# Optimization experiments

Measured on AMD Instinct MI355X. Metric: run time of the kernel, lower is better.

## Reference

```python
import jax, jax.numpy as jnp
import numpy as np
from jax import lax

# hyperparams (match init_kwargs)
DIM = 192      # dim
QK = 192       # qk_dim
HEADS = 8
GS = 128       # group_size
MLP = 384      # mlp_dim
M = 64         # num_tokens
B, H, W = 4, 128, 128


def setup_inputs() -> dict:
    key = jax.random.key(0)
    ks = jax.random.split(key, 12)
    def n(k, sh, sc=0.02):
        return jax.random.normal(k, sh, dtype=jnp.float32) * sc
    return {
        "x": n(ks[0], (B, DIM, H, W), 1.0),
        "ln_g": jnp.ones((DIM,), jnp.float32),
        "ln_b": jnp.zeros((DIM,), jnp.float32),
        "Wq": n(ks[1], (DIM, QK)),
        "Wk": n(ks[2], (DIM, QK)),
        "Wv": n(ks[3], (DIM, DIM)),
        "Wproj": n(ks[4], (DIM, DIM)),
        "Wkg": n(ks[5], (DIM, QK)),      # IRCA global-key projection of means
        "Wvg": n(ks[6], (DIM, DIM)),     # IRCA global-value projection of means
        "means": n(ks[7], (M, DIM), 1.0),  # token dictionary buffer
        "Wconv": n(ks[8], (DIM, DIM)),   # 1x1 conv (no bias) as matrix
        "mlp_ln_g": jnp.ones((DIM,), jnp.float32),
        "mlp_ln_b": jnp.zeros((DIM,), jnp.float32),
        "W_fc1": n(ks[9], (DIM, MLP)),
        "dw": n(ks[10], (MLP, 1, 3, 3)),  # depthwise 3x3 in ConvFFN
        "W_fc2": n(ks[11], (MLP, DIM)),
    }


def _ln(x, g, b, eps=1e-5):
    mu = x.mean(-1, keepdims=True)
    var = ((x - mu) ** 2).mean(-1, keepdims=True)
    return (x - mu) * lax.rsqrt(var + eps) * g + b


def _attn(q, k, v):
    scale = q.shape[-1] ** -0.5
    s = jnp.einsum('...qd,...kd->...qk', q, k) * scale
    p = jax.nn.softmax(s, axis=-1)
    return jnp.einsum('...qk,...kd->...qd', p, v)


def reference(x, ln_g, ln_b, Wq, Wk, Wv, Wproj, Wkg, Wvg, means,
              Wconv, mlp_ln_g, mlp_ln_b, W_fc1, dw, W_fc2):
    b, C, h, w = x.shape
    N = h * w
    xt = x.reshape(b, C, N).transpose(0, 2, 1)          # b n c
    residual = xt
    xn = _ln(xt, ln_g, ln_b)

    # IRCA: per-head global K/V from the token dictionary (means)
    kg = (means @ Wkg).reshape(M, HEADS, QK // HEADS).transpose(1, 0, 2)   # h m dq
    vg = (means @ Wvg).reshape(M, HEADS, C // HEADS).transpose(1, 0, 2)    # h m dv

    # cluster assignment (no-grad): cosine sim to means, argsort by cluster id
    xs = lax.stop_gradient(xn)
    ms = lax.stop_gradient(means)
    xs_n = xs / (jnp.linalg.norm(xs, axis=-1, keepdims=True) + 1e-12)
    ms_n = ms / (jnp.linalg.norm(ms, axis=-1, keepdims=True) + 1e-12)
    belong = jnp.argmax(xs_n @ ms_n.T, axis=-1)          # b n
    idx = jnp.argsort(belong, axis=-1)                   # b n, cluster-sorted order

    # IASA: project, gather into cluster-sorted order
    q = jnp.take_along_axis(xn @ Wq, idx[:, :, None], axis=1)
    k = jnp.take_along_axis(xn @ Wk, idx[:, :, None], axis=1)
    v = jnp.take_along_axis(xn @ Wv, idx[:, :, None], axis=1)

    gs = min(N, GS)
    ng = (N + gs - 1) // gs
    pad_n = ng * gs - N
    pq = jnp.concatenate([q, q[:, N - pad_n:N][:, ::-1]], axis=1)
    pq = pq.reshape(b, ng, gs, HEADS, -1).transpose(0, 1, 3, 2, 4)  # b ng h gs dq

    def windows(t):
        tr = jnp.concatenate([t, t[:, N - pad_n - gs:N][:, ::-1]], axis=1)  # len ng*gs+gs
        t1 = tr[:, :ng * gs].reshape(b, ng, gs, -1)
        t2 = tr[:, gs:].reshape(b, ng, gs, -1)
        tw = jnp.concatenate([t1, t2], axis=2)           # b ng 2gs c
        return tw.reshape(b, ng, 2 * gs, HEADS, -1).transpose(0, 1, 3, 2, 4)

    kw, vw = windows(k), windows(v)
    out1 = _attn(pq, kw, vw)                             # local overlapping windows
    out2 = _attn(pq, kg[None, None], vg[None, None])     # global dictionary attention
    out = (out1 + out2).transpose(0, 1, 3, 2, 4).reshape(b, ng * gs, C)[:, :N]

    # scatter back to original token order (idx is a permutation)
    inv = jnp.argsort(idx, axis=-1)
    out = jnp.take_along_axis(out, inv[:, :, None], axis=1)
    out = (out @ Wproj) @ Wconv                           # proj + 1x1 conv (no bias)
    xt = residual + out

    # PreNorm ConvFFN: LN -> fc1 -> depthwise 3x3 -> GELU -> fc2, residual
    h1 = _ln(xt, mlp_ln_g, mlp_ln_b) @ W_fc1              # b n mlp
    himg = h1.transpose(0, 2, 1).reshape(b, MLP, h, w)
    dwc = lax.conv_general_dilated(himg, dw, (1, 1), 'SAME',
                                   feature_group_count=MLP,
                                   dimension_numbers=('NCHW', 'OIHW', 'NCHW'))
    h2 = jax.nn.gelu(dwc.reshape(b, MLP, N).transpose(0, 2, 1))
    xt = xt + h2 @ W_fc2
    return xt.transpose(0, 2, 1).reshape(b, C, h, w)
```

## Files before the change

### kernel.cpp

```cpp
#include <hip/hip_runtime.h>

using u16 = unsigned short;
using u32 = unsigned int;
typedef __attribute__((ext_vector_type(8))) short short8;
typedef __attribute__((ext_vector_type(4))) short s16x4;
typedef __attribute__((ext_vector_type(4))) float f32x4;
typedef __attribute__((ext_vector_type(2))) float f32x2;
typedef __attribute__((ext_vector_type(4))) u16 u16x4;
typedef __attribute__((ext_vector_type(4))) u32 u32x4;

constexpr int CB   = 4;
constexpr int CC   = 192;
constexpr int CN   = 16384;
constexpr int BN   = CB * CN;
constexpr int CMLP = 384;

__device__ __forceinline__ float b2f(u16 u){ return __uint_as_float(((u32)u) << 16); }
__device__ __forceinline__ u16 f2b(float f){
  u32 u = __float_as_uint(f);
  u32 r = (u + 0x7FFFu + ((u >> 16) & 1u)) >> 16;
  return (u16)r;
}
__device__ __forceinline__ short8 ld8(const u16* p) {
  s16x4 a = *(const s16x4*)p;
  s16x4 b = *(const s16x4*)(p + 4);
  short8 r;
  r[0]=a[0]; r[1]=a[1]; r[2]=a[2]; r[3]=a[3];
  r[4]=b[0]; r[5]=b[1]; r[6]=b[2]; r[7]=b[3];
  return r;
}
__device__ __forceinline__ u32 pk_bf16(float lo, float hi) {
  u32 r;
  asm("v_cvt_pk_bf16_f32 %0, %1, %2" : "=v"(r) : "v"(lo), "v"(hi));
  return r;
}
__device__ __forceinline__ float exp2_fast(float x) {
  float r;
  asm("v_exp_f32 %0, %1" : "=v"(r) : "v"(x));
  return r;
}
__device__ __forceinline__ void gl_lds16(const u16* g, u16* l) {
  __builtin_amdgcn_global_load_lds(
      (const __attribute__((address_space(1))) void*)(const void*)g,
      (__attribute__((address_space(3))) void*)(void*)l, 16, 0, 0);
}

template<int DOARG>
__global__ __launch_bounds__(256) void ln_k(const float* __restrict__ src,
    const float* __restrict__ gg, const float* __restrict__ bb, u16* __restrict__ out,
    const u16* __restrict__ msnT, int* __restrict__ belong)
{
  __shared__ float t[64 * 193];
  __shared__ float sg[192], sb[192];
  __shared__ float smu[64], srs[64];
  const int tid = threadIdx.x;
  const int blk = blockIdx.x;
  const int b = blk >> 8;
  const int n0 = (blk & 255) * 64;
  if (tid < 192) { sg[tid] = gg[tid]; sb[tid] = bb[tid]; }
  const size_t sbase = ((size_t)b * CC) * CN + n0;
  #pragma unroll
  for (int it = 0; it < 48; ++it) {
    int c = it * 4 + (tid >> 6);
    int tok = tid & 63;
    t[tok * 193 + c] = src[sbase + (size_t)c * CN + tok];
  }
  __syncthreads();
  {
    int tok = tid >> 2, sub = tid & 3;
    float s = 0.f, sq = 0.f;
    #pragma unroll
    for (int i = 0; i < 48; ++i) {
      float v = t[tok * 193 + sub * 48 + i];
      s += v; sq += v * v;
    }
    s  += __shfl_xor(s, 1);  s  += __shfl_xor(s, 2);
    sq += __shfl_xor(sq, 1); sq += __shfl_xor(sq, 2);
    float mu = s * (1.f / 192.f);
    float var = fmaxf(sq * (1.f / 192.f) - mu * mu, 0.f);
    float rs = rsqrtf(var + 1e-5f);
    if (sub == 0) { smu[tok] = mu; srs[tok] = rs; }
  }
  __syncthreads();
  const size_t obase = ((size_t)(b * CN + n0)) * CC;
  #pragma unroll
  for (int it = 0; it < 48; ++it) {
    int e = it * 256 + tid;
    int tk = e / 192, c = e % 192;
    float v = (t[tk * 193 + c] - smu[tk]) * srs[tk] * sg[c] + sb[c];
    out[obase + (size_t)tk * CC + c] = f2b(v);
  }

  if (DOARG) {
    const int wv = tid >> 6, lane = tid & 63;
    const int l15 = lane & 15, g4 = lane >> 4, q8 = g4 * 8;
    const int tok = wv * 16 + l15;
    const float mu = smu[tok], rs = srs[tok];
    short8 afm[6];
    #pragma unroll
    for (int ks = 0; ks < 6; ++ks) {
      u32x4 qq;
      #pragma unroll
      for (int j = 0; j < 4; ++j) {
        int c = ks * 32 + q8 + 2 * j;
        float v0 = (t[tok * 193 + c]     - mu) * rs * sg[c]     + sb[c];
        float v1 = (t[tok * 193 + c + 1] - mu) * rs * sg[c + 1] + sb[c + 1];
        qq[j] = pk_bf16(v0, v1);
      }
      afm[ks] = __builtin_bit_cast(short8, qq);
    }
    f32x4 sacc[4];
    #pragma unroll
    for (int ct = 0; ct < 4; ++ct) {
      sacc[ct] = 0.f;
      const u16* pM = msnT + (ct * 16 + l15) * 192 + q8;
      short8 mf[6];
      #pragma unroll
      for (int ks = 0; ks < 6; ++ks) mf[ks] = *(const short8*)(pM + ks * 32);
      #pragma unroll
      for (int ks = 0; ks < 6; ++ks)
        sacc[ct] = __builtin_amdgcn_mfma_f32_16x16x32_bf16(afm[ks], mf[ks], sacc[ct], 0, 0, 0);
    }
    #pragma unroll
    for (int r = 0; r < 4; ++r) {
      float bv = -3e38f; int bi = 1 << 30;
      #pragma unroll
      for (int ct = 0; ct < 4; ++ct) {
        float v = sacc[ct][r];
        int ci = ct * 16 + l15;
        if (v > bv || (v == bv && ci < bi)) { bv = v; bi = ci; }
      }
      #pragma unroll
      for (int d = 1; d < 16; d <<= 1) {
        float ov = __shfl_xor(bv, d);
        int   oi = __shfl_xor(bi, d);
        if (ov > bv || (ov == bv && oi < bi)) { bv = ov; bi = oi; }
      }
      if (l15 == 0) belong[b * CN + n0 + wv * 16 + g4 * 4 + r] = bi;
    }
  }
}

__global__ __launch_bounds__(192) void prep_means_k(const float* __restrict__ means,
    const float* __restrict__ Wkg, const float* __restrict__ Wvg,
    u16* __restrict__ msnT, float* __restrict__ kg, float* __restrict__ vg)
{
  __shared__ float sv[192];
  __shared__ float red[192];
  const int m = blockIdx.x, c = threadIdx.x;
  float v = means[m * 192 + c];
  sv[c] = v; red[c] = v * v;
  __syncthreads();
  for (int s = 96; s >= 3; s >>= 1) {
    if (c < s) red[c] += red[c + s];
    __syncthreads();
  }
  if (c == 0) red[0] = 1.f / (sqrtf(red[0] + red[1] + red[2]) + 1e-12f);
  __syncthreads();
  float scale = red[0];
  msnT[m * 192 + c] = f2b(v * scale);
  float a1 = 0.f, a2 = 0.f;
  for (int cc = 0; cc < 192; ++cc) {
    float mv = sv[cc];
    a1 += mv * Wkg[cc * 192 + c];
    a2 += mv * Wvg[cc * 192 + c];
  }
  int h = c / 24, d = c % 24;
  kg[h * (64 * 24) + m * 24 + d] = a1;
  vg[h * (64 * 24) + m * 24 + d] = a2;
}

__global__ __launch_bounds__(256) void wprep_k(
    const float* __restrict__ Wp, const float* __restrict__ Wc, u16* __restrict__ WpcT,
    const float* __restrict__ Wq, const float* __restrict__ Wk, const float* __restrict__ Wv,
    u16* __restrict__ WqkvT,
    const float* __restrict__ Wfc1, u16* __restrict__ Wfc1T,
    const float* __restrict__ Wfc2, u16* __restrict__ Wfc2T)
{
  int blk = blockIdx.x;
  int tid = threadIdx.x;
  if (blk < 144) {
    int e = blk * 256 + tid;
    if (e < 192 * 192) {
      int i = e / 192, j = e % 192;
      float a = 0.f;
      for (int k = 0; k < 192; ++k) a += Wp[i * 192 + k] * Wc[k * 192 + j];
      WpcT[j * 192 + i] = f2b(a);
    }
    return;
  }
  blk -= 144;
  if (blk < 432) {
    int which = blk / 144;
    int e = (blk % 144) * 256 + tid;
    const float* W = (which == 0) ? Wq : (which == 1) ? Wk : Wv;
    if (e < 192 * 192) {
      int j = e / 192, k = e % 192;
      WqkvT[which * 192 * 192 + e] = f2b(W[k * 192 + j]);
    }
    return;
  }
  blk -= 432;
  if (blk < 288) {
    int e = blk * 256 + tid;
    if (e < 192 * 384) {
      int j = e / 192, k = e % 192;
      Wfc1T[e] = f2b(Wfc1[k * 384 + j]);
    }
    return;
  }
  blk -= 288;
  {
    int e = blk * 256 + tid;
    if (e < 384 * 192) {
      int j = e / 384, k = e % 384;
      Wfc2T[e] = f2b(Wfc2[k * 192 + j]);
    }
  }
}

enum { EP_QKV = 0, EP_RESID = 2, EP_H1 = 3, EP_FINAL = 4 };

template<int KTOT, int NCOLS, int EPI>
__global__ __launch_bounds__(256) void gemm3_k(const u16* __restrict__ A,
    const u16* __restrict__ Wt, const void* __restrict__ residp,
    void* __restrict__ outp, int astride,
    const float* __restrict__ g2, const float* __restrict__ b2, u16* __restrict__ ln2out)
{
  constexpr bool LNB = (EPI == EP_RESID);
  constexpr size_t SH_BYTES = LNB ? (size_t)(64 * 197 * 4) : (size_t)(64 * 192 * 2);
  __shared__ __attribute__((aligned(16))) char shraw[SH_BYTES];
  __shared__ float smu2[64], srs2[64];
  u16*   lA    = (u16*)shraw;
  float* lnbuf = (float*)shraw;
  constexpr int KC = KTOT / 192;
  constexpr int WCOLS = NCOLS / 4;
  constexpr int WCT = WCOLS / 16;
  constexpr int NACC = (KC == 2) ? WCT * 4 : 4;
  const int tid = threadIdx.x;
  const int row0 = blockIdx.y * 64;
  const int b = row0 >> 14;
  const int col0 = blockIdx.x * NCOLS;
  const int wv = tid >> 6, lane = tid & 63;
  const int l15 = lane & 15, g4 = lane >> 4, q8 = g4 * 8;
  const int colw = col0 + wv * WCOLS;

  f32x4 acc[NACC];
  #pragma unroll
  for (int i = 0; i < NACC; ++i) acc[i] = 0.f;

  #pragma unroll
  for (int kc = 0; kc < KC; ++kc) {
    if (kc) __syncthreads();
    #pragma unroll
    for (int j = 0; j < 6; ++j) {
      int C = (wv * 6 + j) * 64 + lane;
      int r = C / 24;
      int c = C - r * 24;
      const u16* gp = A + (size_t)(row0 + r) * astride + kc * 192 + c * 8;
      gl_lds16(gp, lA + (wv * 6 + j) * 512);
    }
    __syncthreads();
    short8 af[4][6];
    #pragma unroll
    for (int rt = 0; rt < 4; ++rt)
      #pragma unroll
      for (int ks = 0; ks < 6; ++ks)
        af[rt][ks] = *(const short8*)(lA + (rt * 16 + l15) * 192 + ks * 32 + q8);
    if (LNB) __syncthreads();

    #pragma unroll
    for (int jc = 0; jc < WCT; ++jc) {
      const u16* pW = Wt + (size_t)(colw + jc * 16 + l15) * KTOT + kc * 192 + q8;
      short8 wf[6];
      #pragma unroll
      for (int ks = 0; ks < 6; ++ks) wf[ks] = *(const short8*)(pW + ks * 32);
      #pragma unroll
      for (int ks = 0; ks < 6; ++ks)
        #pragma unroll
        for (int rt = 0; rt < 4; ++rt) {
          int ai = (KC == 2) ? jc * 4 + rt : rt;
          if (EPI == EP_FINAL || EPI == EP_RESID)
            acc[ai] = __builtin_amdgcn_mfma_f32_16x16x32_bf16(wf[ks], af[rt][ks], acc[ai], 0, 0, 0);
          else
            acc[ai] = __builtin_amdgcn_mfma_f32_16x16x32_bf16(af[rt][ks], wf[ks], acc[ai], 0, 0, 0);
        }

      if (KC == 1 && EPI == EP_QKV) {
        u16* o = (u16*)outp;
        int col = colw + jc * 16 + l15;
        #pragma unroll
        for (int rt = 0; rt < 4; ++rt) {
          int row = row0 + rt * 16 + g4 * 4;
          #pragma unroll
          for (int r = 0; r < 4; ++r)
            o[(size_t)(row + r) * 576 + col] = f2b(acc[rt][r]);
          acc[rt] = 0.f;
        }
      } else if (KC == 1 && EPI == EP_H1) {
        u16* o = (u16*)outp;
        int col = colw + jc * 16 + l15;
        #pragma unroll
        for (int rt = 0; rt < 4; ++rt) {
          int row = row0 + rt * 16 + g4 * 4;
          #pragma unroll
          for (int r = 0; r < 4; ++r)
            o[(size_t)(row + r) * CMLP + col] = f2b(acc[rt][r]);
          acc[rt] = 0.f;
        }
      } else if (KC == 1 && EPI == EP_RESID) {
        const float* resid = (const float*)residp;
        u16* o = (u16*)outp;
        #pragma unroll
        for (int rt = 0; rt < 4; ++rt) {
          int n = ((row0 + rt * 16) & 16383) + l15;
          #pragma unroll
          for (int r = 0; r < 4; ++r) {
            int col = colw + jc * 16 + g4 * 4 + r;
            size_t o2 = ((size_t)(b * CC + col)) * CN + n;
            float val = resid[o2] + acc[rt][r];
            o[o2] = f2b(val);
            lnbuf[(rt * 16 + l15) * 197 + col] = val;
          }
          acc[rt] = 0.f;
        }
      }
    }
  }

  if (EPI == EP_RESID) {
    __syncthreads();
    {
      int tok = tid >> 2, sub = tid & 3;
      float s = 0.f, sq = 0.f;
      #pragma unroll
      for (int i = 0; i < 48; ++i) {
        float v = lnbuf[tok * 197 + sub * 48 + i];
        s += v; sq += v * v;
      }
      s  += __shfl_xor(s, 1);  s  += __shfl_xor(s, 2);
      sq += __shfl_xor(sq, 1); sq += __shfl_xor(sq, 2);
      float mu = s * (1.f / 192.f);
      float var = fmaxf(sq * (1.f / 192.f) - mu * mu, 0.f);
      float rs = rsqrtf(var + 1e-5f);
      if (sub == 0) { smu2[tok] = mu; srs2[tok] = rs; }
    }
    __syncthreads();
    const size_t obase = (size_t)row0 * CC;
    #pragma unroll
    for (int it = 0; it < 48; ++it) {
      int e = it * 256 + tid;
      int tk = e / 192, c = e % 192;
      float v = (lnbuf[tk * 197 + c] - smu2[tk]) * srs2[tk] * g2[c] + b2[c];
      ln2out[obase + (size_t)tk * CC + c] = f2b(v);
    }
  } else if (EPI == EP_FINAL) {
    const u16* resid = (const u16*)residp;
    float* o = (float*)outp;
    #pragma unroll
    for (int jc = 0; jc < WCT; ++jc)
      #pragma unroll
      for (int tt = 0; tt < 4; ++tt) {
        int n = ((row0 + tt * 16) & 16383) + l15;
        #pragma unroll
        for (int r = 0; r < 4; ++r) {
          int outcol = colw + jc * 16 + g4 * 4 + r;
          size_t o2 = ((size_t)(b * CC + outcol)) * CN + n;
          o[o2] = b2f(resid[o2]) + acc[jc * 4 + tt][r];
        }
      }
  }
}

__global__ __launch_bounds__(256) void hist_k(const int* __restrict__ belong, int* __restrict__ histG)
{
  __shared__ int h[64];
  int tid = threadIdx.x, blk = blockIdx.x;
  if (tid < 64) h[tid] = 0;
  __syncthreads();
  int c = belong[blk * 256 + tid];
  atomicAdd(&h[c], 1);
  __syncthreads();
  if (tid < 64) histG[blk * 64 + tid] = h[tid];
}

__global__ __launch_bounds__(64) void scan_k(const int* __restrict__ histG, int* __restrict__ chunkBase)
{
  int b = blockIdx.x, c = threadIdx.x;
  int tot = 0;
  for (int ch = 0; ch < 64; ++ch) tot += histG[(b * 64 + ch) * 64 + c];
  int inc = tot;
  for (int d = 1; d < 64; d <<= 1) {
    int v = __shfl_up(inc, d);
    if (c >= d) inc += v;
  }
  int run = inc - tot;
  for (int ch = 0; ch < 64; ++ch) {
    chunkBase[(b * 64 + ch) * 64 + c] = run;
    run += histG[(b * 64 + ch) * 64 + c];
  }
}

__global__ __launch_bounds__(256) void rank_k(const int* __restrict__ belong,
    const int* __restrict__ chunkBase, int* __restrict__ idx)
{
  __shared__ int WH[4][64];
  int tid = threadIdx.x, blk = blockIdx.x;
  int b = blk >> 6, chl = blk & 63;
  int wv = tid >> 6, lane = tid & 63;
  ((int*)WH)[tid] = 0;
  __syncthreads();
  int nl = chl * 256 + tid;
  int c = belong[blk * 256 + tid];
  int rank = 0;
  for (int m = 0; m < 64; ++m) {
    unsigned long long msk = __ballot(c == m);
    if (c == m) {
      rank = __popcll(msk & ((1ull << lane) - 1ull));
      if (rank == 0) WH[wv][m] = __popcll(msk);
    }
  }
  __syncthreads();
  int off = 0;
  #pragma unroll
  for (int w = 0; w < 3; ++w) if (w < wv) off += WH[w][c];
  int pos = chunkBase[(b * 64 + chl) * 64 + c] + off + rank;
  idx[b * CN + pos] = nl;
}

__global__ __launch_bounds__(256) void attn_k(u16* __restrict__ qkv,
    const float* __restrict__ kg, const float* __restrict__ vg,
    const int* __restrict__ idx)
{
  __shared__ __attribute__((aligned(16))) u16 sK[320 * 24];
  __shared__ __attribute__((aligned(16))) u16 sVT[25 * 332];
  __shared__ u16 sidx[256];
  const int g = blockIdx.x, h = blockIdx.y, b = blockIdx.z;
  const int tid = threadIdx.x;
  const int wave = tid >> 6, lane = tid & 63;
  const int l15 = lane & 15, g4 = lane >> 4;
  const int q8 = g4 * 8;
  const size_t base = (size_t)b * CN * 576;
  const float QSC = 0.20412414523193154f * 1.4426950408889634f;
  short8 z8 = {0,0,0,0,0,0,0,0};

  {
    int p = g * 128 + tid;
    if (p >= CN) p = 2 * CN - 1 - p;
    sidx[tid] = (u16)idx[b * CN + p];
  }
  for (int e = tid; e < 332; e += 256) sVT[24 * 332 + e] = 0x3F80;
  __syncthreads();

  #pragma unroll
  for (int it = 0; it < 8; ++it) {
    int e4 = (it * 256 + tid) * 4;
    if (e4 < 7680) {
      int r = e4 / 24, c = e4 % 24;
      if (r < 256) {
        int p = sidx[r];
        *(u16x4*)(sK + r * 24 + c) =
          *(const u16x4*)(qkv + base + (size_t)p * 576 + 192 + h * 24 + c);
      } else {
        const float* kp = kg + h * 1536 + (r - 256) * 24 + c;
        u16x4 o;
        o[0] = f2b(kp[0]); o[1] = f2b(kp[1]); o[2] = f2b(kp[2]); o[3] = f2b(kp[3]);
        *(u16x4*)(sK + r * 24 + c) = o;
      }
    }
  }
  #pragma unroll
  for (int it = 0; it < 8; ++it) {
    int e4 = (it * 256 + tid) * 4;
    if (e4 < 7680) {
      int kk = e4 / 24, c = e4 % 24;
      if (kk < 256) {
        int p = sidx[kk];
        u16x4 v = *(const u16x4*)(qkv + base + (size_t)p * 576 + 384 + h * 24 + c);
        sVT[(c + 0) * 332 + kk] = v[0];
        sVT[(c + 1) * 332 + kk] = v[1];
        sVT[(c + 2) * 332 + kk] = v[2];
        sVT[(c + 3) * 332 + kk] = v[3];
      } else {
        const float* vp = vg + h * 1536 + (kk - 256) * 24 + c;
        sVT[(c + 0) * 332 + kk] = f2b(vp[0]);
        sVT[(c + 1) * 332 + kk] = f2b(vp[1]);
        sVT[(c + 2) * 332 + kk] = f2b(vp[2]);
        sVT[(c + 3) * 332 + kk] = f2b(vp[3]);
      }
    }
  }

  short8 qf[2];
  #pragma unroll
  for (int rt = 0; rt < 2; ++rt) {
    int qrow = sidx[wave * 32 + rt * 16 + l15];
    if (g4 < 3) {
      short8 raw = ld8(qkv + base + (size_t)qrow * 576 + h * 24 + q8);
      u32x4 qq;
      #pragma unroll
      for (int j = 0; j < 4; ++j) {
        float lo = b2f((u16)raw[2 * j]) * QSC;
        float hi = b2f((u16)raw[2 * j + 1]) * QSC;
        qq[j] = pk_bf16(lo, hi);
      }
      qf[rt] = __builtin_bit_cast(short8, qq);
    } else {
      qf[rt] = z8;
    }
  }
  __syncthreads();

  f32x4 O1[2][2], O2[2][2];
  #pragma unroll
  for (int rt = 0; rt < 2; ++rt)
    #pragma unroll
    for (int ct2 = 0; ct2 < 2; ++ct2) { O1[rt][ct2] = 0.f; O2[rt][ct2] = 0.f; }

  const int srcLo = ((lane & 16) << 1) + l15;
  const int srcHi = srcLo + 16;
  const bool hiSel = lane >= 32;
  f32x4 zz = 0.f;

  auto do_tile = [&](int ktile, f32x4 (*O)[2]) {
    short8 aK[4];
    #pragma unroll
    for (int ct = 0; ct < 4; ++ct)
      aK[ct] = (g4 < 3) ? ld8(sK + (ktile + ct * 16 + l15) * 24 + q8) : z8;
    short8 bV[2][2];
    #pragma unroll
    for (int kc = 0; kc < 2; ++kc)
      #pragma unroll
      for (int ct2 = 0; ct2 < 2; ++ct2) {
        int vrow = ct2 * 16 + l15;
        bV[kc][ct2] = (vrow < 25) ? ld8(sVT + vrow * 332 + ktile + kc * 32 + q8) : z8;
      }
    #pragma unroll
    for (int rt = 0; rt < 2; ++rt) {
      f32x4 p[4];
      __builtin_amdgcn_s_setprio(1);
      #pragma unroll
      for (int ct = 0; ct < 4; ++ct)
        p[ct] = __builtin_amdgcn_mfma_f32_16x16x32_bf16(aK[ct], qf[rt], zz, 0, 0, 0);
      __builtin_amdgcn_s_setprio(0);
      #pragma unroll
      for (int ct = 0; ct < 4; ++ct)
        #pragma unroll
        for (int r = 0; r < 4; ++r)
          p[ct][r] = exp2_fast(p[ct][r]);
      #pragma unroll
      for (int kc = 0; kc < 2; ++kc) {
        u32 wA0 = pk_bf16(p[kc * 2][0], p[kc * 2][1]);
        u32 wA1 = pk_bf16(p[kc * 2][2], p[kc * 2][3]);
        u32 wB0 = pk_bf16(p[kc * 2 + 1][0], p[kc * 2 + 1][1]);
        u32 wB1 = pk_bf16(p[kc * 2 + 1][2], p[kc * 2 + 1][3]);
        u32 a0 = (u32)__shfl((int)wA0, srcLo), a1 = (u32)__shfl((int)wA1, srcLo);
        u32 a2 = (u32)__shfl((int)wA0, srcHi), a3 = (u32)__shfl((int)wA1, srcHi);
        u32 b0 = (u32)__shfl((int)wB0, srcLo), b1 = (u32)__shfl((int)wB1, srcLo);
        u32 b2 = (u32)__shfl((int)wB0, srcHi), b3 = (u32)__shfl((int)wB1, srcHi);
        u32x4 fr;
        fr[0] = hiSel ? b0 : a0; fr[1] = hiSel ? b1 : a1;
        fr[2] = hiSel ? b2 : a2; fr[3] = hiSel ? b3 : a3;
        short8 aP = __builtin_bit_cast(short8, fr);
        __builtin_amdgcn_s_setprio(1);
        #pragma unroll
        for (int ct2 = 0; ct2 < 2; ++ct2)
          O[rt][ct2] = __builtin_amdgcn_mfma_f32_16x16x32_bf16(aP, bV[kc][ct2], O[rt][ct2], 0, 0, 0);
        __builtin_amdgcn_s_setprio(0);
      }
    }
  };

  do_tile(0,   O1);
  do_tile(64,  O1);
  do_tile(128, O1);
  do_tile(192, O1);
  do_tile(256, O2);

  const int lsrc = (lane & 48) + 8;
  #pragma unroll
  for (int rt = 0; rt < 2; ++rt) {
    #pragma unroll
    for (int r = 0; r < 4; ++r) {
      float s1 = __shfl(O1[rt][1][r], lsrc);
      float s2 = __shfl(O2[rt][1][r], lsrc);
      float i1 = 1.f / s1;
      float i2 = 1.f / s2;
      int tok = sidx[wave * 32 + rt * 16 + g4 * 4 + r];
      #pragma unroll
      for (int ct2 = 0; ct2 < 2; ++ct2) {
        int d = ct2 * 16 + l15;
        if (d < 24) {
          float v = O1[rt][ct2][r] * i1 + O2[rt][ct2][r] * i2;
          qkv[base + (size_t)tok * 576 + h * 24 + d] = f2b(v);
        }
      }
    }
  }
}

__global__ __launch_bounds__(256) void conv_k(const u16* __restrict__ h1,
    const float* __restrict__ dw, u16* __restrict__ h2g)
{
  __shared__ float t[1156 * 10];
  __shared__ float sdw[72];
  const int tile = blockIdx.x;
  const int jg = blockIdx.y;
  const int bb = blockIdx.z;
  const int y0 = (tile >> 2) * 32, x0 = (tile & 3) * 32;
  const int tid = threadIdx.x;
  if (tid < 72) sdw[tid] = dw[jg * 72 + tid];
  #pragma unroll
  for (int it = 0; it < 5; ++it) {
    int e = it * 256 + tid;
    if (e < 1156) {
      int yy = e / 34 - 1 + y0, xx = e % 34 - 1 + x0;
      float v[8];
      if (yy >= 0 && yy < 128 && xx >= 0 && xx < 128) {
        short8 raw = *(const short8*)(h1 + ((size_t)(bb * CN + yy * 128 + xx)) * CMLP + jg * 8);
        #pragma unroll
        for (int c = 0; c < 8; ++c) v[c] = b2f((u16)raw[c]);
      } else {
        #pragma unroll
        for (int c = 0; c < 8; ++c) v[c] = 0.f;
      }
      #pragma unroll
      for (int c = 0; c < 8; c += 2) {
        f32x2 p; p[0] = v[c]; p[1] = v[c + 1];
        *(f32x2*)(t + e * 10 + c) = p;
      }
    }
  }
  __syncthreads();
  float acc[4][8];
  #pragma unroll
  for (int px = 0; px < 4; ++px)
    #pragma unroll
    for (int c = 0; c < 8; ++c) acc[px][c] = 0.f;
  #pragma unroll
  for (int k = 0; k < 9; ++k) {
    const int dy = k / 3, dx = k % 3;
    float w[8];
    #pragma unroll
    for (int c = 0; c < 8; ++c) w[c] = sdw[c * 9 + k];
    #pragma unroll
    for (int px = 0; px < 4; ++px) {
      int idx2 = px * 256 + tid;
      int oy = idx2 >> 5, ox = idx2 & 31;
      const float* vp = t + ((oy + dy) * 34 + ox + dx) * 10;
      #pragma unroll
      for (int c = 0; c < 8; ++c) acc[px][c] += vp[c] * w[c];
    }
  }
  #pragma unroll
  for (int px = 0; px < 4; ++px) {
    int idx2 = px * 256 + tid;
    int oy = idx2 >> 5, ox = idx2 & 31;
    short8 o;
    #pragma unroll
    for (int c = 0; c < 8; ++c) {
      float a = acc[px][c];
      float u = 1.5957691216057308f * (a + 0.044715f * a * a * a);
      float gel = a / (1.f + __expf(-u));
      o[c] = (short)f2b(gel);
    }
    *(short8*)(h2g + ((size_t)(bb * CN + (y0 + oy) * 128 + x0 + ox)) * CMLP + jg * 8) = o;
  }
}

extern "C" void kernel_launch(void* const* d_in, const int* in_sizes, int n_in,
                              void* d_out, int out_size, void* d_ws, size_t ws_size,
                              hipStream_t stream)
{
  const float* x     = (const float*)d_in[0];
  const float* ln_g  = (const float*)d_in[1];
  const float* ln_b  = (const float*)d_in[2];
  const float* Wq    = (const float*)d_in[3];
  const float* Wk    = (const float*)d_in[4];
  const float* Wv    = (const float*)d_in[5];
  const float* Wproj = (const float*)d_in[6];
  const float* Wkg   = (const float*)d_in[7];
  const float* Wvg   = (const float*)d_in[8];
  const float* means = (const float*)d_in[9];
  const float* Wconv = (const float*)d_in[10];
  const float* mlp_g = (const float*)d_in[11];
  const float* mlp_b = (const float*)d_in[12];
  const float* Wfc1  = (const float*)d_in[13];
  const float* dw    = (const float*)d_in[14];
  const float* Wfc2  = (const float*)d_in[15];
  float* out = (float*)d_out;
  (void)in_sizes; (void)n_in; (void)out_size; (void)ws_size;

  char* ws = (char*)d_ws;
  size_t off = 0;
  auto alloc = [&](size_t sz) { void* p = ws + off; off += (sz + 255) & ~(size_t)255; return p; };
  u16*  xn    = (u16*)alloc((size_t)BN * 192 * 2);
  u16*  qkv   = (u16*)alloc((size_t)BN * 576 * 2);
  u16*  xt2   = (u16*)alloc((size_t)BN * 192 * 2);
  u16*  h2g   = (u16*)alloc((size_t)BN * 384 * 2);
  u16*  msnT  = (u16*)alloc(64 * 192 * 2);
  u16*  WqkvT = (u16*)alloc(576 * 192 * 2);
  u16*  WpcT  = (u16*)alloc(192 * 192 * 2);
  u16*  Wfc1T = (u16*)alloc(384 * 192 * 2);
  u16*  Wfc2T = (u16*)alloc(192 * 384 * 2);
  float* kg   = (float*)alloc(8 * 64 * 24 * 4);
  float* vg   = (float*)alloc(8 * 64 * 24 * 4);
  int*  belong = (int*)alloc(BN * 4);
  int*  idxb   = (int*)alloc(BN * 4);
  int*  histG  = (int*)alloc(256 * 64 * 4);
  int*  chunkBase = (int*)alloc(256 * 64 * 4);
  u16* ln2 = xn;
  u16* h1  = qkv;

  prep_means_k<<<64, 192, 0, stream>>>(means, Wkg, Wvg, msnT, kg, vg);
  wprep_k<<<1152, 256, 0, stream>>>(Wproj, Wconv, WpcT, Wq, Wk, Wv, WqkvT,
                                    Wfc1, Wfc1T, Wfc2, Wfc2T);

  ln_k<1><<<1024, 256, 0, stream>>>(x, ln_g, ln_b, xn, msnT, belong);
  hist_k<<<256, 256, 0, stream>>>(belong, histG);
  scan_k<<<4, 64, 0, stream>>>(histG, chunkBase);
  rank_k<<<256, 256, 0, stream>>>(belong, chunkBase, idxb);
  gemm3_k<192, 576, EP_QKV><<<dim3(1, 1024), 256, 0, stream>>>(xn, WqkvT, nullptr, qkv, 192, nullptr, nullptr, nullptr);
  attn_k<<<dim3(128, 8, 4), 256, 0, stream>>>(qkv, kg, vg, idxb);
  gemm3_k<192, 192, EP_RESID><<<dim3(1, 1024), 256, 0, stream>>>(qkv, WpcT, x, xt2, 576, mlp_g, mlp_b, ln2);
  gemm3_k<192, 384, EP_H1><<<dim3(1, 1024), 256, 0, stream>>>(ln2, Wfc1T, nullptr, h1, 192, nullptr, nullptr, nullptr);
  conv_k<<<dim3(16, 48, 4), 256, 0, stream>>>(h1, dw, h2g);
  gemm3_k<384, 192, EP_FINAL><<<dim3(1, 1024), 256, 0, stream>>>(h2g, Wfc2T, xt2, out, 384, nullptr, nullptr, nullptr);
}
```

Before: 319.1 us.

## Fuse LN into QKV GEMM and proj/residual/LN2 into fc1 GEMM

The first LayerNorm kernel now computes the QKV projection directly from its register-resident normalized fragments, so the bf16 normalized activation is no longer written to and reread from global memory. The proj+residual kernel now runs LN2 in shared memory and immediately does the fc1 GEMM, removing the LN2 round trip and one launch. This cuts two kernel launches and roughly two full activation round trips. In exchange, the LN2 statistics are computed from bf16-rounded residual values instead of fp32, and each wave in the QKV step does far more serial MFMA work per block, with weights streamed from global memory.

```diff
diff --git a/kernel.cpp b/kernel.cpp
--- a/kernel.cpp
+++ b/kernel.cpp
@@ -45,10 +45,10 @@
       (__attribute__((address_space(3))) void*)(void*)l, 16, 0, 0);
 }
 
-template<int DOARG>
-__global__ __launch_bounds__(256) void ln_k(const float* __restrict__ src,
-    const float* __restrict__ gg, const float* __restrict__ bb, u16* __restrict__ out,
-    const u16* __restrict__ msnT, int* __restrict__ belong)
+__global__ __launch_bounds__(256) void lnqkv_k(const float* __restrict__ src,
+    const float* __restrict__ gg, const float* __restrict__ bb,
+    const u16* __restrict__ msnT, const u16* __restrict__ WqkvT,
+    int* __restrict__ belong, u16* __restrict__ qkv)
 {
   __shared__ float t[64 * 193];
   __shared__ float sg[192], sb[192];
@@ -82,33 +82,26 @@
     if (sub == 0) { smu[tok] = mu; srs[tok] = rs; }
   }
   __syncthreads();
-  const size_t obase = ((size_t)(b * CN + n0)) * CC;
-  #pragma unroll
-  for (int it = 0; it < 48; ++it) {
-    int e = it * 256 + tid;
-    int tk = e / 192, c = e % 192;
-    float v = (t[tk * 193 + c] - smu[tk]) * srs[tk] * sg[c] + sb[c];
-    out[obase + (size_t)tk * CC + c] = f2b(v);
-  }
-
-  if (DOARG) {
-    const int wv = tid >> 6, lane = tid & 63;
-    const int l15 = lane & 15, g4 = lane >> 4, q8 = g4 * 8;
-    const int tok = wv * 16 + l15;
-    const float mu = smu[tok], rs = srs[tok];
-    short8 afm[6];
-    #pragma unroll
-    for (int ks = 0; ks < 6; ++ks) {
-      u32x4 qq;
-      #pragma unroll
-      for (int j = 0; j < 4; ++j) {
-        int c = ks * 32 + q8 + 2 * j;
-        float v0 = (t[tok * 193 + c]     - mu) * rs * sg[c]     + sb[c];
-        float v1 = (t[tok * 193 + c + 1] - mu) * rs * sg[c + 1] + sb[c + 1];
-        qq[j] = pk_bf16(v0, v1);
-      }
-      afm[ks] = __builtin_bit_cast(short8, qq);
-    }
+
+  const int wv = tid >> 6, lane = tid & 63;
+  const int l15 = lane & 15, g4 = lane >> 4, q8 = g4 * 8;
+  const int tok = wv * 16 + l15;
+  const float mu = smu[tok], rs = srs[tok];
+  short8 afm[6];
+  #pragma unroll
+  for (int ks = 0; ks < 6; ++ks) {
+    u32x4 qq;
+    #pragma unroll
+    for (int j = 0; j < 4; ++j) {
+      int c = ks * 32 + q8 + 2 * j;
+      float v0 = (t[tok * 193 + c]     - mu) * rs * sg[c]     + sb[c];
+      float v1 = (t[tok * 193 + c + 1] - mu) * rs * sg[c + 1] + sb[c + 1];
+      qq[j] = pk_bf16(v0, v1);
+    }
+    afm[ks] = __builtin_bit_cast(short8, qq);
+  }
+
+  {
     f32x4 sacc[4];
     #pragma unroll
     for (int ct = 0; ct < 4; ++ct) {
@@ -138,6 +131,23 @@
       }
       if (l15 == 0) belong[b * CN + n0 + wv * 16 + g4 * 4 + r] = bi;
     }
+  }
+
+  const size_t rowb = (size_t)(b * CN + n0 + wv * 16 + g4 * 4);
+  #pragma unroll 4
+  for (int jc = 0; jc < 36; ++jc) {
+    const u16* pW = WqkvT + (size_t)(jc * 16 + l15) * 192 + q8;
+    short8 wf[6];
+    #pragma unroll
+    for (int ks = 0; ks < 6; ++ks) wf[ks] = *(const short8*)(pW + ks * 32);
+    f32x4 acc = 0.f;
+    #pragma unroll
+    for (int ks = 0; ks < 6; ++ks)
+      acc = __builtin_amdgcn_mfma_f32_16x16x32_bf16(afm[ks], wf[ks], acc, 0, 0, 0);
+    int col = jc * 16 + l15;
+    #pragma unroll
+    for (int r = 0; r < 4; ++r)
+      qkv[(rowb + r) * 576 + col] = f2b(acc[r]);
   }
 }
 
@@ -219,35 +229,145 @@
   }
 }
 
-enum { EP_QKV = 0, EP_RESID = 2, EP_H1 = 3, EP_FINAL = 4 };
-
-template<int KTOT, int NCOLS, int EPI>
-__global__ __launch_bounds__(256) void gemm3_k(const u16* __restrict__ A,
-    const u16* __restrict__ Wt, const void* __restrict__ residp,
-    void* __restrict__ outp, int astride,
-    const float* __restrict__ g2, const float* __restrict__ b2, u16* __restrict__ ln2out)
-{
-  constexpr bool LNB = (EPI == EP_RESID);
-  constexpr size_t SH_BYTES = LNB ? (size_t)(64 * 197 * 4) : (size_t)(64 * 192 * 2);
-  __shared__ __attribute__((aligned(16))) char shraw[SH_BYTES];
+__global__ __launch_bounds__(256) void resid_k(const u16* __restrict__ qkv,
+    const u16* __restrict__ WpcT, const float* __restrict__ x, u16* __restrict__ xt2,
+    const float* __restrict__ g2, const float* __restrict__ b2,
+    const u16* __restrict__ Wfc1T, u16* __restrict__ h1)
+{
+  __shared__ __attribute__((aligned(16))) u16 shraw[64 * 200];
   __shared__ float smu2[64], srs2[64];
-  u16*   lA    = (u16*)shraw;
-  float* lnbuf = (float*)shraw;
+  u16* lA    = shraw;
+  u16* lnb16 = shraw;
+  const int tid = threadIdx.x;
+  const int row0 = blockIdx.x * 64;
+  const int b = row0 >> 14;
+  const int wv = tid >> 6, lane = tid & 63;
+  const int l15 = lane & 15, g4 = lane >> 4, q8 = g4 * 8;
+
+  #pragma unroll
+  for (int j = 0; j < 6; ++j) {
+    int C = (wv * 6 + j) * 64 + lane;
+    int r = C / 24;
+    int c = C - r * 24;
+    const u16* gp = qkv + (size_t)(row0 + r) * 576 + c * 8;
+    gl_lds16(gp, lA + (wv * 6 + j) * 512);
+  }
+  __syncthreads();
+  short8 af[4][6];
+  #pragma unroll
+  for (int rt = 0; rt < 4; ++rt)
+    #pragma unroll
+    for (int ks = 0; ks < 6; ++ks)
+      af[rt][ks] = *(const short8*)(lA + (rt * 16 + l15) * 192 + ks * 32 + q8);
+  __syncthreads();
+
+  const int colw = wv * 48;
+  #pragma unroll
+  for (int jc = 0; jc < 3; ++jc) {
+    const u16* pW = WpcT + (size_t)(colw + jc * 16 + l15) * 192 + q8;
+    short8 wf[6];
+    #pragma unroll
+    for (int ks = 0; ks < 6; ++ks) wf[ks] = *(const short8*)(pW + ks * 32);
+    f32x4 acc[4];
+    #pragma unroll
+    for (int rt = 0; rt < 4; ++rt) acc[rt] = 0.f;
+    #pragma unroll
+    for (int ks = 0; ks < 6; ++ks)
+      #pragma unroll
+      for (int rt = 0; rt < 4; ++rt)
+        acc[rt] = __builtin_amdgcn_mfma_f32_16x16x32_bf16(wf[ks], af[rt][ks], acc[rt], 0, 0, 0);
+    #pragma unroll
+    for (int rt = 0; rt < 4; ++rt) {
+      int n = ((row0 + rt * 16) & 16383) + l15;
+      #pragma unroll
+      for (int r = 0; r < 4; ++r) {
+        int col = colw + jc * 16 + g4 * 4 + r;
+        size_t o2 = ((size_t)(b * CC + col)) * CN + n;
+        float val = x[o2] + acc[rt][r];
+        u16 vb = f2b(val);
+        xt2[o2] = vb;
+        lnb16[(rt * 16 + l15) * 200 + col] = vb;
+      }
+    }
+  }
+  __syncthreads();
+
+  {
+    int tok = tid >> 2, sub = tid & 3;
+    float s = 0.f, sq = 0.f;
+    #pragma unroll
+    for (int i = 0; i < 48; ++i) {
+      float v = b2f(lnb16[tok * 200 + sub * 48 + i]);
+      s += v; sq += v * v;
+    }
+    s  += __shfl_xor(s, 1);  s  += __shfl_xor(s, 2);
+    sq += __shfl_xor(sq, 1); sq += __shfl_xor(sq, 2);
+    float mu = s * (1.f / 192.f);
+    float var = fmaxf(sq * (1.f / 192.f) - mu * mu, 0.f);
+    float rs = rsqrtf(var + 1e-5f);
+    if (sub == 0) { smu2[tok] = mu; srs2[tok] = rs; }
+  }
+  __syncthreads();
+  #pragma unroll
+  for (int it = 0; it < 48; ++it) {
+    int e = it * 256 + tid;
+    int tk = e / 192, c = e % 192;
+    float v = (b2f(lnb16[tk * 200 + c]) - smu2[tk]) * srs2[tk] * g2[c] + b2[c];
+    lnb16[tk * 200 + c] = f2b(v);
+  }
+  __syncthreads();
+
+  short8 af2[4][6];
+  #pragma unroll
+  for (int rt = 0; rt < 4; ++rt)
+    #pragma unroll
+    for (int ks = 0; ks < 6; ++ks)
+      af2[rt][ks] = *(const short8*)(lnb16 + (rt * 16 + l15) * 200 + ks * 32 + q8);
+  const int colw2 = wv * 96;
+  #pragma unroll
+  for (int jc = 0; jc < 6; ++jc) {
+    const u16* pW = Wfc1T + (size_t)(colw2 + jc * 16 + l15) * 192 + q8;
+    short8 wf[6];
+    #pragma unroll
+    for (int ks = 0; ks < 6; ++ks) wf[ks] = *(const short8*)(pW + ks * 32);
+    f32x4 acc[4];
+    #pragma unroll
+    for (int rt = 0; rt < 4; ++rt) acc[rt] = 0.f;
+    #pragma unroll
+    for (int ks = 0; ks < 6; ++ks)
+      #pragma unroll
+      for (int rt = 0; rt < 4; ++rt)
+        acc[rt] = __builtin_amdgcn_mfma_f32_16x16x32_bf16(af2[rt][ks], wf[ks], acc[rt], 0, 0, 0);
+    int col = colw2 + jc * 16 + l15;
+    #pragma unroll
+    for (int rt = 0; rt < 4; ++rt) {
+      int row = row0 + rt * 16 + g4 * 4;
+      #pragma unroll
+      for (int r = 0; r < 4; ++r)
+        h1[(size_t)(row + r) * CMLP + col] = f2b(acc[rt][r]);
+    }
+  }
+}
+
+template<int KTOT, int NCOLS>
+__global__ __launch_bounds__(256) void gemmF_k(const u16* __restrict__ A,
+    const u16* __restrict__ Wt, const u16* __restrict__ resid,
+    float* __restrict__ o, int astride)
+{
+  __shared__ __attribute__((aligned(16))) u16 lA[64 * 192];
   constexpr int KC = KTOT / 192;
   constexpr int WCOLS = NCOLS / 4;
   constexpr int WCT = WCOLS / 16;
-  constexpr int NACC = (KC == 2) ? WCT * 4 : 4;
   const int tid = threadIdx.x;
-  const int row0 = blockIdx.y * 64;
+  const int row0 = blockIdx.x * 64;
   const int b = row0 >> 14;
-  const int col0 = blockIdx.x * NCOLS;
   const int wv = tid >> 6, lane = tid & 63;
   const int l15 = lane & 15, g4 = lane >> 4, q8 = g4 * 8;
-  const int colw = col0 + wv * WCOLS;
-
-  f32x4 acc[NACC];
-  #pragma unroll
-  for (int i = 0; i < NACC; ++i) acc[i] = 0.f;
+  const int colw = wv * WCOLS;
+
+  f32x4 acc[WCT * 4];
+  #pragma unroll
+  for (int i = 0; i < WCT * 4; ++i) acc[i] = 0.f;
 
   #pragma unroll
   for (int kc = 0; kc < KC; ++kc) {
@@ -267,7 +387,6 @@
       #pragma unroll
       for (int ks = 0; ks < 6; ++ks)
         af[rt][ks] = *(const short8*)(lA + (rt * 16 + l15) * 192 + ks * 32 + q8);
-    if (LNB) __syncthreads();
 
     #pragma unroll
     for (int jc = 0; jc < WCT; ++jc) {
@@ -278,98 +397,22 @@
       #pragma unroll
       for (int ks = 0; ks < 6; ++ks)
         #pragma unroll
-        for (int rt = 0; rt < 4; ++rt) {
-          int ai = (KC == 2) ? jc * 4 + rt : rt;
-          if (EPI == EP_FINAL || EPI == EP_RESID)
-            acc[ai] = __builtin_amdgcn_mfma_f32_16x16x32_bf16(wf[ks], af[rt][ks], acc[ai], 0, 0, 0);
-          else
-            acc[ai] = __builtin_amdgcn_mfma_f32_16x16x32_bf16(af[rt][ks], wf[ks], acc[ai], 0, 0, 0);
-        }
-
-      if (KC == 1 && EPI == EP_QKV) {
-        u16* o = (u16*)outp;
-        int col = colw + jc * 16 + l15;
-        #pragma unroll
-        for (int rt = 0; rt < 4; ++rt) {
-          int row = row0 + rt * 16 + g4 * 4;
-          #pragma unroll
-          for (int r = 0; r < 4; ++r)
-            o[(size_t)(row + r) * 576 + col] = f2b(acc[rt][r]);
-          acc[rt] = 0.f;
-        }
-      } else if (KC == 1 && EPI == EP_H1) {
-        u16* o = (u16*)outp;
-        int col = colw + jc * 16 + l15;
-        #pragma unroll
-        for (int rt = 0; rt < 4; ++rt) {
-          int row = row0 + rt * 16 + g4 * 4;
-          #pragma unroll
-          for (int r = 0; r < 4; ++r)
-            o[(size_t)(row + r) * CMLP + col] = f2b(acc[rt][r]);
-          acc[rt] = 0.f;
-        }
-      } else if (KC == 1 && EPI == EP_RESID) {
-        const float* resid = (const float*)residp;
-        u16* o = (u16*)outp;
-        #pragma unroll
-        for (int rt = 0; rt < 4; ++rt) {
-          int n = ((row0 + rt * 16) & 16383) + l15;
-          #pragma unroll
-          for (int r = 0; r < 4; ++r) {
-            int col = colw + jc * 16 + g4 * 4 + r;
-            size_t o2 = ((size_t)(b * CC + col)) * CN + n;
-            float val = resid[o2] + acc[rt][r];
-            o[o2] = f2b(val);
-            lnbuf[(rt * 16 + l15) * 197 + col] = val;
-          }
-          acc[rt] = 0.f;
-        }
-      }
-    }
-  }
-
-  if (EPI == EP_RESID) {
-    __syncthreads();
-    {
-      int tok = tid >> 2, sub = tid & 3;
-      float s = 0.f, sq = 0.f;
-      #pragma unroll
-      for (int i = 0; i < 48; ++i) {
-        float v = lnbuf[tok * 197 + sub * 48 + i];
-        s += v; sq += v * v;
-      }
-      s  += __shfl_xor(s, 1);  s  += __shfl_xor(s, 2);
-      sq += __shfl_xor(sq, 1); sq += __shfl_xor(sq, 2);
-      float mu = s * (1.f / 192.f);
-      float var = fmaxf(sq * (1.f / 192.f) - mu * mu, 0.f);
-      float rs = rsqrtf(var + 1e-5f);
-      if (sub == 0) { smu2[tok] = mu; srs2[tok] = rs; }
-    }
-    __syncthreads();
-    const size_t obase = (size_t)row0 * CC;
-    #pragma unroll
-    for (int it = 0; it < 48; ++it) {
-      int e = it * 256 + tid;
-      int tk = e / 192, c = e % 192;
-      float v = (lnbuf[tk * 197 + c] - smu2[tk]) * srs2[tk] * g2[c] + b2[c];
-      ln2out[obase + (size_t)tk * CC + c] = f2b(v);
-    }
-  } else if (EPI == EP_FINAL) {
-    const u16* resid = (const u16*)residp;
-    float* o = (float*)outp;
-    #pragma unroll
-    for (int jc = 0; jc < WCT; ++jc)
-      #pragma unroll
-      for (int tt = 0; tt < 4; ++tt) {
-        int n = ((row0 + tt * 16) & 16383) + l15;
-        #pragma unroll
-        for (int r = 0; r < 4; ++r) {
-          int outcol = colw + jc * 16 + g4 * 4 + r;
-          size_t o2 = ((size_t)(b * CC + outcol)) * CN + n;
-          o[o2] = b2f(resid[o2]) + acc[jc * 4 + tt][r];
-        }
-      }
-  }
+        for (int rt = 0; rt < 4; ++rt)
+          acc[jc * 4 + rt] = __builtin_amdgcn_mfma_f32_16x16x32_bf16(wf[ks], af[rt][ks], acc[jc * 4 + rt], 0, 0, 0);
+    }
+  }
+  #pragma unroll
+  for (int jc = 0; jc < WCT; ++jc)
+    #pragma unroll
+    for (int tt = 0; tt < 4; ++tt) {
+      int n = ((row0 + tt * 16) & 16383) + l15;
+      #pragma unroll
+      for (int r = 0; r < 4; ++r) {
+        int outcol = colw + jc * 16 + g4 * 4 + r;
+        size_t o2 = ((size_t)(b * CC + outcol)) * CN + n;
+        o[o2] = b2f(resid[o2]) + acc[jc * 4 + tt][r];
+      }
+    }
 }
 
 __global__ __launch_bounds__(256) void hist_k(const int* __restrict__ belong, int* __restrict__ histG)
@@ -694,9 +737,9 @@
   char* ws = (char*)d_ws;
   size_t off = 0;
   auto alloc = [&](size_t sz) { void* p = ws + off; off += (sz + 255) & ~(size_t)255; return p; };
-  u16*  xn    = (u16*)alloc((size_t)BN * 192 * 2);
   u16*  qkv   = (u16*)alloc((size_t)BN * 576 * 2);
   u16*  xt2   = (u16*)alloc((size_t)BN * 192 * 2);
+  u16*  h1    = (u16*)alloc((size_t)BN * 384 * 2);
   u16*  h2g   = (u16*)alloc((size_t)BN * 384 * 2);
   u16*  msnT  = (u16*)alloc(64 * 192 * 2);
   u16*  WqkvT = (u16*)alloc(576 * 192 * 2);
@@ -709,21 +752,17 @@
   int*  idxb   = (int*)alloc(BN * 4);
   int*  histG  = (int*)alloc(256 * 64 * 4);
   int*  chunkBase = (int*)alloc(256 * 64 * 4);
-  u16* ln2 = xn;
-  u16* h1  = qkv;
 
   prep_means_k<<<64, 192, 0, stream>>>(means, Wkg, Wvg, msnT, kg, vg);
   wprep_k<<<1152, 256, 0, stream>>>(Wproj, Wconv, WpcT, Wq, Wk, Wv, WqkvT,
                                     Wfc1, Wfc1T, Wfc2, Wfc2T);
 
-  ln_k<1><<<1024, 256, 0, stream>>>(x, ln_g, ln_b, xn, msnT, belong);
+  lnqkv_k<<<1024, 256, 0, stream>>>(x, ln_g, ln_b, msnT, WqkvT, belong, qkv);
   hist_k<<<256, 256, 0, stream>>>(belong, histG);
   scan_k<<<4, 64, 0, stream>>>(histG, chunkBase);
   rank_k<<<256, 256, 0, stream>>>(belong, chunkBase, idxb);
-  gemm3_k<192, 576, EP_QKV><<<dim3(1, 1024), 256, 0, stream>>>(xn, WqkvT, nullptr, qkv, 192, nullptr, nullptr, nullptr);
   attn_k<<<dim3(128, 8, 4), 256, 0, stream>>>(qkv, kg, vg, idxb);
-  gemm3_k<192, 192, EP_RESID><<<dim3(1, 1024), 256, 0, stream>>>(qkv, WpcT, x, xt2, 576, mlp_g, mlp_b, ln2);
-  gemm3_k<192, 384, EP_H1><<<dim3(1, 1024), 256, 0, stream>>>(ln2, Wfc1T, nullptr, h1, 192, nullptr, nullptr, nullptr);
+  resid_k<<<1024, 256, 0, stream>>>(qkv, WpcT, x, xt2, mlp_g, mlp_b, Wfc1T, h1);
   conv_k<<<dim3(16, 48, 4), 256, 0, stream>>>(h1, dw, h2g);
-  gemm3_k<384, 192, EP_FINAL><<<dim3(1, 1024), 256, 0, stream>>>(h2g, Wfc2T, xt2, out, 384, nullptr, nullptr, nullptr);
-}
+  gemmF_k<384, 192><<<1024, 256, 0, stream>>>(h2g, Wfc2T, xt2, out, 384);
+}
```

Result: slower. 347.4 us (+8.9%).
